# Kernel tuning notes

Hardware: AMD Instinct MI355X
Metric: run time of the kernel (lower is better)

## Reference

```python
import jax, jax.numpy as jnp
import numpy as np

V, D, H, HD, L, T, B = 65, 384, 6, 64, 6, 256, 64
EPS = 1e-3  # keras LayerNormalization default epsilon


def setup_inputs() -> dict:
    key = jax.random.key(0)
    ks = jax.random.split(key, 12)
    s = 0.02
    n = lambda k, shp: jax.random.normal(k, shp, dtype=jnp.float32) * s
    return {
        "idx": jax.random.randint(ks[0], (B, T), 0, V),
        "tok_emb": n(ks[1], (V, D)),
        "pos_emb": n(ks[2], (T, D)),
        "Wq": n(ks[3], (L, H, D, HD)),
        "Wk": n(ks[4], (L, H, D, HD)),
        "Wv": n(ks[5], (L, H, D, HD)),
        "Wproj": n(ks[6], (L, D, D)),
        "bproj": jnp.zeros((L, D), jnp.float32),
        "W1": n(ks[7], (L, D, 4 * D)),
        "b1": jnp.zeros((L, 4 * D), jnp.float32),
        "W2": n(ks[8], (L, 4 * D, D)),
        "b2": jnp.zeros((L, D), jnp.float32),
        "ln1_g": jnp.ones((L, D), jnp.float32),
        "ln1_b": jnp.zeros((L, D), jnp.float32),
        "ln2_g": jnp.ones((L, D), jnp.float32),
        "ln2_b": jnp.zeros((L, D), jnp.float32),
        "lnf_g": jnp.ones((D,), jnp.float32),
        "lnf_b": jnp.zeros((D,), jnp.float32),
        "Whead": n(ks[9], (D, V)),
        "bhead": jnp.zeros((V,), jnp.float32),
    }


def _ln(x, g, b):
    m = jnp.mean(x, axis=-1, keepdims=True)
    v = jnp.mean(jnp.square(x - m), axis=-1, keepdims=True)
    return (x - m) * jax.lax.rsqrt(v + EPS) * g + b


def reference(idx, tok_emb, pos_emb, Wq, Wk, Wv, Wproj, bproj, W1, b1, W2, b2,
              ln1_g, ln1_b, ln2_g, ln2_b, lnf_g, lnf_b, Whead, bhead):
    Bn, Tn = idx.shape
    x = tok_emb[idx] + pos_emb[:Tn]  # [B,T,D]
    mask = jnp.tril(jnp.ones((Tn, Tn), dtype=bool))
    scale = jnp.float32(D) ** -0.5  # NOTE: original scales by full C=n_embd, not head_size
    for l in range(L):
        h = _ln(x, ln1_g[l], ln1_b[l])
        q = jnp.einsum('btd,hdk->bhtk', h, Wq[l])
        k = jnp.einsum('btd,hdk->bhtk', h, Wk[l])
        v = jnp.einsum('btd,hdk->bhtk', h, Wv[l])
        wei = jnp.einsum('bhtk,bhsk->bhts', q, k) * scale
        wei = jnp.where(mask, wei, -jnp.inf)
        wei = jax.nn.softmax(wei, axis=-1)
        att = jnp.einsum('bhts,bhsk->bhtk', wei, v)
        att = att.transpose(0, 2, 1, 3).reshape(Bn, Tn, D)  # concat heads
        x = x + att @ Wproj[l] + bproj[l]
        h2 = _ln(x, ln2_g[l], ln2_b[l])
        x = x + jax.nn.relu(h2 @ W1[l] + b1[l]) @ W2[l] + b2[l]
    x = _ln(x, lnf_g, lnf_b)
    return x @ Whead + bhead  # logits [B,T,V]
```

## Files before the change

kernel.cpp:

```cpp
#include <hip/hip_runtime.h>
#include <hip/hip_bf16.h>

#define B_  64
#define T_  256
#define D_  384
#define H_  6
#define HD_ 64
#define L_  6
#define V_  65
#define BT  (B_*T_)

typedef __hip_bfloat16 bf16;
typedef unsigned short u16;
typedef short s16;
typedef __attribute__((ext_vector_type(8))) short bf16x8;
typedef __attribute__((ext_vector_type(4))) float f32x4;

#define OFF_QKV   0
#define OFF_PROJ  442368
#define OFF_W1T   589824
#define OFF_W2T   1179648
#define OFF_BPROJ 1769472
#define OFF_B1    1769856
#define OFF_B2    1771392
#define OFF_LN1G  1771776
#define OFF_LN1B  1772160
#define OFF_LN2G  1772544
#define OFF_LN2B  1772928
#define WBUF_E    1773312
#define HOFF_WHT  0
#define HOFF_BH   24960
#define HOFF_LNFG 25088
#define HOFF_LNFB 25472
#define HBUF_E    25856

__device__ __forceinline__ float u2f(u16 u) {
  union { unsigned i; float f; } c; c.i = ((unsigned)u) << 16; return c.f;
}
__device__ __forceinline__ bf16 f2b(float x) { return __float2bfloat16(x); }
__device__ __forceinline__ float b2f(bf16 x) { return __bfloat162float(x); }
__device__ __forceinline__ u16 f2u(float x) { bf16 h = f2b(x); return *(u16*)&h; }

__device__ __forceinline__ float pload(const void* p, size_t i, bool f32w) {
  return f32w ? ((const float*)p)[i] : u2f(((const u16*)p)[i]);
}

__device__ __forceinline__ void swz(int gid, int ntc, int mtiles,
                                    int& nt, int& mblk) {
  if ((mtiles & 7) == 0) {
    int per = ntc << 3;
    int g   = gid / per;
    int rem = gid - g * per;
    nt   = rem >> 3;
    mblk = (g << 3) + (rem & 7);
  } else {
    nt   = gid / mtiles;
    mblk = gid - nt * mtiles;
  }
}

__global__ __launch_bounds__(256) void detect_kernel(
    const void* p1,  const void* p2,  const void* p3,  const void* p4,
    const void* p5,  const void* p6,  const void* p7,  const void* p8,
    const void* p9,  const void* p10, const void* p11, const void* p12,
    const void* p13, const void* p14, const void* p15, const void* p16,
    const void* p17, const void* p18, const void* p19,
    const int* __restrict__ idx, unsigned* flags)
{
  const void* ps[20] = {nullptr, p1, p2, p3, p4, p5, p6, p7, p8, p9, p10,
                        p11, p12, p13, p14, p15, p16, p17, p18, p19};
  const int esz[20] = {16384, 24960, 98304, 884736, 884736, 884736, 884736,
                       2304, 3538944, 9216, 3538944, 2304, 2304, 2304, 2304,
                       2304, 384, 384, 24960, 65};
  __shared__ int r1[256], r2[256];
  int bid = blockIdx.x, tid = threadIdx.x;
  if (bid == 19) {
    int z = 0;
    for (int m = tid; m < 4096; m += 256) z += (idx[2 * m + 1] == 0) ? 1 : 0;
    r1[tid] = z; __syncthreads();
    for (int s = 128; s > 0; s >>= 1) {
      if (tid < s) r1[tid] += r1[tid + s];
      __syncthreads();
    }
    if (tid == 0) flags[20] = (r1[0] >= 4000) ? 1u : 0u;
    return;
  }
  int j = bid + 1;
  const u16* p = (const u16*)ps[j];
  int ns = esz[j] / 2; if (ns > 1024) ns = 1024;
  int band = 0, nz = 0;
  for (int i = tid; i < ns; i += 256) {
    u16 lo = p[2 * i], hi = p[2 * i + 1];
    int e = (lo >> 7) & 0xFF;
    band += (e >= 100 && e <= 127) ? 1 : 0;
    nz   += (lo | hi) ? 1 : 0;
  }
  r1[tid] = band; r2[tid] = nz; __syncthreads();
  for (int s = 128; s > 0; s >>= 1) {
    if (tid < s) { r1[tid] += r1[tid + s]; r2[tid] += r2[tid + s]; }
    __syncthreads();
  }
  if (tid == 0) flags[j] = (r2[0] > 0 && r1[0] * 2 < ns) ? 1u : 0u;
}

__global__ void const_kernel(float* out, int n, float val) {
  int i = blockIdx.x * 256 + threadIdx.x;
  if (i < n) out[i] = val;
}

__global__ __launch_bounds__(256) void conv_layer(
    const void* Wq, const void* Wk, const void* Wv, const void* Wproj,
    const void* bproj, const void* W1, const void* b1, const void* W2,
    const void* b2, const void* ln1g, const void* ln1b, const void* ln2g,
    const void* ln2b, const unsigned* __restrict__ flags,
    bf16* __restrict__ dst, int l)
{
  int e = blockIdx.x * 256 + threadIdx.x;
  if (e >= WBUF_E) return;
  float v;
  if (e < OFF_PROJ) {
    int math = e / 24576;
    int rem  = e - math * 24576;
    int hd = rem / 384, d = rem - hd * 384;
    int mat = math / 6, hh = math - mat * 6;
    const void* src = (mat == 0 ? Wq : mat == 1 ? Wk : Wv);
    v = pload(src, ((size_t)(l * 6 + hh) * 384 + d) * 64 + hd, flags[3 + mat] != 0);
  } else if (e < OFF_W1T) {
    int e2 = e - OFF_PROJ;
    int n = e2 / 384, d = e2 - n * 384;
    v = pload(Wproj, ((size_t)l * 384 + d) * 384 + n, flags[6] != 0);
  } else if (e < OFF_W2T) {
    int e2 = e - OFF_W1T;
    int n = e2 / 384, d = e2 - n * 384;
    v = pload(W1, ((size_t)l * 384 + d) * 1536 + n, flags[8] != 0);
  } else if (e < OFF_BPROJ) {
    int e2 = e - OFF_W2T;
    int n = e2 / 1536, k = e2 - n * 1536;
    v = pload(W2, ((size_t)l * 1536 + k) * 384 + n, flags[10] != 0);
  } else {
    int e2 = e - OFF_BPROJ;
    if      (e2 < 384)  v = pload(bproj, (size_t)l * 384 + e2, flags[7] != 0);
    else if (e2 < 1920) v = pload(b1, (size_t)l * 1536 + (e2 - 384), flags[9] != 0);
    else if (e2 < 2304) v = pload(b2, (size_t)l * 384 + (e2 - 1920), flags[11] != 0);
    else if (e2 < 2688) v = pload(ln1g, (size_t)l * 384 + (e2 - 2304), flags[12] != 0);
    else if (e2 < 3072) v = pload(ln1b, (size_t)l * 384 + (e2 - 2688), flags[13] != 0);
    else if (e2 < 3456) v = pload(ln2g, (size_t)l * 384 + (e2 - 3072), flags[14] != 0);
    else                v = pload(ln2b, (size_t)l * 384 + (e2 - 3456), flags[15] != 0);
  }
  dst[e] = f2b(v);
}

__global__ __launch_bounds__(256) void conv_head(
    const void* Wh, const void* bh, const void* lnfg, const void* lnfb,
    const unsigned* __restrict__ flags, bf16* __restrict__ dst)
{
  int e = blockIdx.x * 256 + threadIdx.x;
  if (e >= HBUF_E) return;
  float v = 0.f;
  if (e < HOFF_BH) {
    int n = e / 384, d = e - n * 384;
    v = pload(Wh, (size_t)d * 65 + n, flags[18] != 0);
  } else if (e < 25025) {
    v = pload(bh, e - HOFF_BH, flags[19] != 0);
  } else if (e < HOFF_LNFG) {
    v = 0.f;
  } else if (e < HOFF_LNFB) {
    v = pload(lnfg, e - HOFF_LNFG, flags[16] != 0);
  } else {
    v = pload(lnfb, e - HOFF_LNFB, flags[17] != 0);
  }
  dst[e] = f2b(v);
}

__global__ __launch_bounds__(256) void embed_kernel(
    const void* __restrict__ idx, const void* __restrict__ tok,
    const void* __restrict__ pos, bf16* __restrict__ x,
    const unsigned* __restrict__ flags)
{
  int i   = blockIdx.x * 256 + threadIdx.x;
  int tkn = i / D_;
  int d   = i - tkn * D_;
  int t   = tkn & (T_ - 1);
  long long tix;
  if (flags[20]) tix = ((const long long*)idx)[tkn];
  else           tix = ((const int*)idx)[tkn];
  float v = pload(tok, (size_t)tix * D_ + d, flags[1] != 0)
          + pload(pos, (size_t)t * D_ + d, flags[2] != 0);
  x[i] = f2b(v);
}

__global__ __launch_bounds__(256) void lnw_kernel(
    const bf16* __restrict__ x, const u16* __restrict__ g,
    const u16* __restrict__ b, bf16* __restrict__ hc, int tok0)
{
  int w = threadIdx.x >> 6, lane = threadIdx.x & 63;
  int lm = blockIdx.x * 4 + w;
  const bf16* xr = x + (size_t)(tok0 + lm) * D_;
  float v[6]; float s = 0.f;
#pragma unroll
  for (int j = 0; j < 6; j++) { v[j] = b2f(xr[lane + 64 * j]); s += v[j]; }
#pragma unroll
  for (int o = 1; o < 64; o <<= 1) s += __shfl_xor(s, o, 64);
  float mean = s * (1.0f / D_);
  float sq = 0.f;
#pragma unroll
  for (int j = 0; j < 6; j++) { float d0 = v[j] - mean; sq += d0 * d0; }
#pragma unroll
  for (int o = 1; o < 64; o <<= 1) sq += __shfl_xor(sq, o, 64);
  float inv = 1.0f / sqrtf(sq * (1.0f / D_) + 1e-3f);
  bf16* hr = hc + (size_t)lm * D_;
#pragma unroll
  for (int j = 0; j < 6; j++) {
    int d = lane + 64 * j;
    hr[d] = f2b((v[j] - mean) * inv * u2f(g[d]) + u2f(b[d]));
  }
}

__device__ __forceinline__ void gll16(const void* g, void* l) {
  __builtin_amdgcn_global_load_lds(
      (const __attribute__((address_space(1))) unsigned*)g,
      (__attribute__((address_space(3))) unsigned*)l, 16, 0, 0);
}

__device__ __forceinline__ bf16x8 ldfrag(const s16* lds, int r, int s) {
  return *(const bf16x8*)(lds + r * 64 + ((s ^ (r & 7)) << 3));
}

template<int NT, class Epi>
__device__ __forceinline__ void mcore(
    s16* __restrict__ As, s16* __restrict__ Wl,
    const u16* __restrict__ A, const u16* __restrict__ WT,
    int N, int K, int arow0, int n0, Epi epi)
{
  constexpr int MREP = (NT == 128) ? 4 : 2;
  constexpr int WPW  = NT / 32;
  int tid = threadIdx.x;
  int w = tid >> 6, lane = tid & 63;
  int quad = lane >> 4, l15 = lane & 15;
  int r8 = lane >> 3;
  int sl = ((lane & 7) ^ r8) * 8;
  int wm = (NT == 128) ? ((w >> 1) * 64) : (w * 32);
  int wn = (NT == 128) ? ((w & 1) * 64) : 0;

  f32x4 acc[MREP][4];
#pragma unroll
  for (int i = 0; i < MREP; i++)
#pragma unroll
    for (int j = 0; j < 4; j++) acc[i][j] = (f32x4){0.f, 0.f, 0.f, 0.f};

  const u16* Ag[4];
#pragma unroll
  for (int i = 0; i < 4; i++)
    Ag[i] = A + (size_t)(arow0 + (w * 4 + i) * 8 + r8) * K + sl;
  const u16* Wg[WPW];
#pragma unroll
  for (int i = 0; i < WPW; i++)
    Wg[i] = WT + (size_t)(n0 + (w * WPW + i) * 8 + r8) * K + sl;

  for (int k0 = 0; k0 < K; k0 += 64) {
    __syncthreads();
#pragma unroll
    for (int i = 0; i < 4; i++)
      gll16(Ag[i] + k0, As + (w * 4 + i) * 512);
#pragma unroll
    for (int i = 0; i < WPW; i++)
      gll16(Wg[i] + k0, Wl + (w * WPW + i) * 512);
    __syncthreads();
#pragma unroll
    for (int kh = 0; kh < 2; kh++) {
      bf16x8 am[MREP], bn[4];
#pragma unroll
      for (int i = 0; i < MREP; i++)
        am[i] = ldfrag(As, wm + i * 16 + l15, kh * 4 + quad);
#pragma unroll
      for (int j = 0; j < 4; j++)
        bn[j] = ldfrag(Wl, wn + j * 16 + l15, kh * 4 + quad);
#pragma unroll
      for (int i = 0; i < MREP; i++)
#pragma unroll
        for (int j = 0; j < 4; j++)
          acc[i][j] = __builtin_amdgcn_mfma_f32_16x16x32_bf16(am[i], bn[j], acc[i][j], 0, 0, 0);
    }
  }

#pragma unroll
  for (int i = 0; i < MREP; i++)
#pragma unroll
    for (int j = 0; j < 4; j++)
#pragma unroll
      for (int r = 0; r < 4; r++) {
        int m = wm + i * 16 + quad * 4 + r;
        int n = n0 + wn + j * 16 + l15;
        if (n < N) epi(m, n, acc[i][j][r]);
      }
}

__global__ __launch_bounds__(256) void qkv128(
    const bf16* hc, const bf16* Wbuf, bf16* qkvc, int MCa, int mtiles)
{
  __shared__ __attribute__((aligned(16))) s16 As[128 * 64];
  __shared__ __attribute__((aligned(16))) s16 Ws[128 * 64];
  int nt, mblk;
  swz(blockIdx.x, 9, mtiles, nt, mblk);
  int n0 = nt * 128, mloc0 = mblk * 128;
  auto epi = [&](int m, int n, float v) {
    int mat = n / 384;
    int rem = n - mat * 384;
    int hh = rem >> 6, hd = rem & 63;
    qkvc[(size_t)mat * MCa * D_ + (size_t)hh * MCa * HD_
         + (size_t)(mloc0 + m) * HD_ + hd] = f2b(v);
  };
  mcore<128>(As, Ws, (const u16*)hc,
             (const u16*)Wbuf + OFF_QKV, 1152, D_, mloc0, n0, epi);
}

__global__ __launch_bounds__(256) void ffn1_128(
    const bf16* hc, const bf16* Wbuf, bf16* midc, int mtiles)
{
  __shared__ __attribute__((aligned(16))) s16 As[128 * 64];
  __shared__ __attribute__((aligned(16))) s16 Ws[128 * 64];
  int nt, mblk;
  swz(blockIdx.x, 12, mtiles, nt, mblk);
  int n0 = nt * 128, m0 = mblk * 128;
  const bf16* bias = (const bf16*)Wbuf + OFF_B1;
  auto epi = [&](int m, int n, float v) {
    float r = v + b2f(bias[n]);
    midc[(size_t)(m0 + m) * (4 * D_) + n] = f2b(fmaxf(r, 0.f));
  };
  mcore<128>(As, Ws, (const u16*)hc,
             (const u16*)Wbuf + OFF_W1T, 4 * D_, D_, m0, n0, epi);
}

__global__ __launch_bounds__(256) void proj_mfma(
    const bf16* A, const bf16* Wbuf, bf16* x, int tok0, int mtiles)
{
  __shared__ __attribute__((aligned(16))) s16 As[128 * 64];
  __shared__ __attribute__((aligned(16))) s16 Ws[64 * 64];
  int nt, mblk;
  swz(blockIdx.x, 6, mtiles, nt, mblk);
  int n0 = nt * 64, m0 = mblk * 128;
  const bf16* bias = (const bf16*)Wbuf + OFF_BPROJ;
  auto epi = [&](int m, int n, float v) {
    size_t o = (size_t)(tok0 + m0 + m) * D_ + n;
    x[o] = f2b(v + b2f(bias[n]) + b2f(x[o]));
  };
  mcore<64>(As, Ws, (const u16*)A,
            (const u16*)Wbuf + OFF_PROJ, D_, D_, m0, n0, epi);
}

__global__ __launch_bounds__(256) void ffn2_mfma(
    const bf16* midc, const bf16* Wbuf, bf16* x, int tok0, int mtiles)
{
  __shared__ __attribute__((aligned(16))) s16 As[128 * 64];
  __shared__ __attribute__((aligned(16))) s16 Ws[64 * 64];
  int nt, mblk;
  swz(blockIdx.x, 6, mtiles, nt, mblk);
  int n0 = nt * 64, m0 = mblk * 128;
  const bf16* bias = (const bf16*)Wbuf + OFF_B2;
  auto epi = [&](int m, int n, float v) {
    size_t o = (size_t)(tok0 + m0 + m) * D_ + n;
    x[o] = f2b(v + b2f(bias[n]) + b2f(x[o]));
  };
  mcore<64>(As, Ws, (const u16*)midc,
            (const u16*)Wbuf + OFF_W2T, D_, 4 * D_, m0, n0, epi);
}

__global__ __launch_bounds__(256) void head_mfma(
    const bf16* hc, const bf16* Hbuf, float* out, int tok0)
{
  __shared__ __attribute__((aligned(16))) s16 As[128 * 64];
  __shared__ __attribute__((aligned(16))) s16 Ws[64 * 64];
  int n0 = blockIdx.x * 64, m0 = blockIdx.y * 128;
  const bf16* bias = (const bf16*)Hbuf + HOFF_BH;
  auto epi = [&](int m, int n, float v) {
    out[(size_t)(tok0 + m0 + m) * V_ + n] = v + b2f(bias[n]);
  };
  mcore<64>(As, Ws, (const u16*)hc,
            (const u16*)Hbuf + HOFF_WHT, V_, D_, m0, n0, epi);
}

__global__ __launch_bounds__(256) void attn4_kernel(
    const bf16* __restrict__ Q, const bf16* __restrict__ K,
    const bf16* __restrict__ V, bf16* __restrict__ att, int MCa)
{
  __shared__ s16 Qs[64 * 72];
  __shared__ s16 Ks[64 * 72];
  __shared__ __attribute__((aligned(16))) s16 Vt[64 * 64];
  __shared__ s16 Ps[4][16 * 72];
  const float scale = 0.05103103630798288f;
  int tid = threadIdx.x;
  int w = tid >> 6, lane = tid & 63;
  int quad = lane >> 4, l15 = lane & 15;
  int bid = blockIdx.x;
  int qt = bid & 3;
  int bh = bid >> 2;
  int b = bh / H_, h = bh - b * H_;
  size_t base = ((size_t)h * MCa + (size_t)b * T_) * HD_;
  int q0 = qt * 64;
  int cq = qt;

  int rstg = (tid & 7) + 8 * (tid >> 6);
  int sstg = (tid >> 3) & 7;

#pragma unroll
  for (int i = 0; i < 2; i++) {
    int r = rstg + 32 * i;
    *(bf16x8*)&Qs[r * 72 + sstg * 8] =
        *(const bf16x8*)((const u16*)Q + base + (size_t)(q0 + r) * HD_ + sstg * 8);
  }

  float mrow[4] = {-1e30f, -1e30f, -1e30f, -1e30f};
  float lrow[4] = {0.f, 0.f, 0.f, 0.f};
  f32x4 O[4];
#pragma unroll
  for (int nt = 0; nt < 4; nt++) O[nt] = (f32x4){0.f, 0.f, 0.f, 0.f};

  for (int c = 0; c <= cq; c++) {
    __syncthreads();
#pragma unroll
    for (int i = 0; i < 2; i++) {
      int r = rstg + 32 * i;
      *(bf16x8*)&Ks[r * 72 + sstg * 8] =
          *(const bf16x8*)((const u16*)K + base + (size_t)(c * 64 + r) * HD_ + sstg * 8);
      bf16x8 vv =
          *(const bf16x8*)((const u16*)V + base + (size_t)(c * 64 + r) * HD_ + sstg * 8);
      int rs = r >> 3, rl = r & 7;
      int so = ((rs ^ sstg) << 3) + rl;
#pragma unroll
      for (int k = 0; k < 8; k++)
        Vt[(sstg * 8 + k) * 64 + so] = vv[k];
    }
    __syncthreads();

    f32x4 S[4];
#pragma unroll
    for (int nt = 0; nt < 4; nt++) S[nt] = (f32x4){0.f, 0.f, 0.f, 0.f};
#pragma unroll
    for (int ks = 0; ks < 2; ks++) {
      int kk = ks * 32 + quad * 8;
      bf16x8 a = *(const bf16x8*)&Qs[(w * 16 + l15) * 72 + kk];
#pragma unroll
      for (int nt = 0; nt < 4; nt++) {
        bf16x8 bb8 = *(const bf16x8*)&Ks[(nt * 16 + l15) * 72 + kk];
        S[nt] = __builtin_amdgcn_mfma_f32_16x16x32_bf16(a, bb8, S[nt], 0, 0, 0);
      }
    }

#pragma unroll
    for (int nt = 0; nt < 4; nt++)
#pragma unroll
      for (int r = 0; r < 4; r++) {
        int qrow = q0 + w * 16 + quad * 4 + r;
        int sg = c * 64 + nt * 16 + l15;
        float v = S[nt][r] * scale;
        S[nt][r] = (sg <= qrow) ? v : -1e30f;
      }

    float alpha[4];
#pragma unroll
    for (int r = 0; r < 4; r++) {
      float mc = fmaxf(fmaxf(S[0][r], S[1][r]), fmaxf(S[2][r], S[3][r]));
#pragma unroll
      for (int o = 1; o < 16; o <<= 1) mc = fmaxf(mc, __shfl_xor(mc, o, 64));
      float mn = fmaxf(mrow[r], mc);
      alpha[r] = __expf(mrow[r] - mn);
      mrow[r] = mn;
      float s = 0.f;
#pragma unroll
      for (int nt = 0; nt < 4; nt++) {
        float p = __expf(S[nt][r] - mn);
        S[nt][r] = p;
        s += p;
      }
#pragma unroll
      for (int o = 1; o < 16; o <<= 1) s += __shfl_xor(s, o, 64);
      lrow[r] = lrow[r] * alpha[r] + s;
    }
#pragma unroll
    for (int nt = 0; nt < 4; nt++)
#pragma unroll
      for (int r = 0; r < 4; r++) O[nt][r] *= alpha[r];

#pragma unroll
    for (int nt = 0; nt < 4; nt++)
#pragma unroll
      for (int r = 0; r < 4; r++)
        Ps[w][(quad * 4 + r) * 72 + nt * 16 + l15] = (s16)f2u(S[nt][r]);
    __syncthreads();
#pragma unroll
    for (int ks = 0; ks < 2; ks++) {
      bf16x8 a = *(const bf16x8*)&Ps[w][l15 * 72 + ks * 32 + quad * 8];
#pragma unroll
      for (int nt = 0; nt < 4; nt++) {
        int d = nt * 16 + l15;
        bf16x8 bb8 = *(const bf16x8*)&Vt[d * 64 +
            (((ks * 4 + quad) ^ ((d >> 3) & 7)) << 3)];
        O[nt] = __builtin_amdgcn_mfma_f32_16x16x32_bf16(a, bb8, O[nt], 0, 0, 0);
      }
    }
  }

#pragma unroll
  for (int r = 0; r < 4; r++) {
    float invl = 1.0f / lrow[r];
#pragma unroll
    for (int nt = 0; nt < 4; nt++) {
      int qrow = q0 + w * 16 + quad * 4 + r;
      att[(size_t)(b * T_ + qrow) * D_ + h * HD_ + nt * 16 + l15] =
          f2b(O[nt][r] * invl);
    }
  }
}

extern "C" void kernel_launch(void* const* d_in, const int* in_sizes, int n_in,
                              void* d_out, int out_size, void* d_ws, size_t ws_size,
                              hipStream_t stream)
{
  float* out = (float*)d_out;
  dim3 blk(256);
  int outg = (out_size + 255) / 256;

  static const int expected[20] = {
      16384, 24960, 98304, 884736, 884736, 884736, 884736, 2304,
      3538944, 9216, 3538944, 2304, 2304, 2304, 2304, 2304, 384, 384,
      24960, 65};
  if (n_in != 20) { const_kernel<<<outg, blk, 0, stream>>>(out, out_size, 5.0f); return; }
  for (int i = 0; i < 20; i++)
    if (in_sizes[i] != expected[i]) {
      const_kernel<<<outg, blk, 0, stream>>>(out, out_size, 10.0f * (i + 1));
      return;
    }
  if (out_size != BT * V_) { const_kernel<<<outg, blk, 0, stream>>>(out, out_size, 7.0f); return; }

  const void* idx   = d_in[0];
  const void* tok   = d_in[1];
  const void* pos   = d_in[2];
  const void* Wq    = d_in[3];
  const void* Wk    = d_in[4];
  const void* Wv    = d_in[5];
  const void* Wproj = d_in[6];
  const void* bproj = d_in[7];
  const void* W1    = d_in[8];
  const void* b1    = d_in[9];
  const void* W2    = d_in[10];
  const void* b2    = d_in[11];
  const void* ln1g  = d_in[12];
  const void* ln1b  = d_in[13];
  const void* ln2g  = d_in[14];
  const void* ln2b  = d_in[15];
  const void* lnfg  = d_in[16];
  const void* lnfb  = d_in[17];
  const void* Whead = d_in[18];
  const void* bhead = d_in[19];

  const size_t off_x  = 256;
  const size_t off_wb = off_x + (size_t)BT * D_ * 2;
  const size_t off_hb = off_wb + (size_t)WBUF_E * 2;
  const size_t fixed  = off_hb + ((size_t)HBUF_E * 2 + 63) / 64 * 64;
  if (ws_size < fixed) {
    const_kernel<<<outg, blk, 0, stream>>>(out, out_size, 0.0f);
    return;
  }
  size_t region = ws_size - fixed;

  int nc = 0;
  const int candn[7] = {1, 2, 4, 8, 16, 32, 64};
  for (int i = 0; i < 7; i++)
    if ((size_t)5 * (BT / candn[i]) * D_ * 2 <= region) { nc = candn[i]; break; }
  if (!nc) { const_kernel<<<outg, blk, 0, stream>>>(out, out_size, 0.0f); return; }
  const int MCc = BT / nc;
  const int CBc = MCc / T_;
  const int mtiles = MCc / 128;

  char* wsb = (char*)d_ws;
  unsigned* flags = (unsigned*)wsb;
  bf16*   x    = (bf16*)(wsb + off_x);
  bf16*   Wbuf = (bf16*)(wsb + off_wb);
  bf16*   Hbuf = (bf16*)(wsb + off_hb);
  bf16*   hc   = (bf16*)(wsb + fixed);
  bf16*   qkvc = hc + (size_t)MCc * D_;
  bf16*   attc = qkvc + (size_t)3 * MCc * D_;
  bf16*   midc = qkvc;

  detect_kernel<<<dim3(20), blk, 0, stream>>>(
      tok, pos, Wq, Wk, Wv, Wproj, bproj, W1, b1, W2, b2,
      ln1g, ln1b, ln2g, ln2b, lnfg, lnfb, Whead, bhead,
      (const int*)idx, flags);
  embed_kernel<<<dim3(BT * D_ / 256), blk, 0, stream>>>(idx, tok, pos, x, flags);
  conv_head<<<dim3((HBUF_E + 255) / 256), blk, 0, stream>>>(
      Whead, bhead, lnfg, lnfb, flags, Hbuf);

  for (int l = 0; l < L_; l++) {
    conv_layer<<<dim3((WBUF_E + 255) / 256), blk, 0, stream>>>(
        Wq, Wk, Wv, Wproj, bproj, W1, b1, W2, b2,
        ln1g, ln1b, ln2g, ln2b, flags, Wbuf, l);
    for (int c = 0; c < nc; c++) {
      int tok0 = c * MCc;
      lnw_kernel<<<dim3(MCc / 4), blk, 0, stream>>>(
          x, (const u16*)Wbuf + OFF_LN1G, (const u16*)Wbuf + OFF_LN1B, hc, tok0);
      qkv128<<<dim3(9 * mtiles), blk, 0, stream>>>(hc, Wbuf, qkvc, MCc, mtiles);
      attn4_kernel<<<dim3(CBc * H_ * 4), blk, 0, stream>>>(
          qkvc, qkvc + (size_t)MCc * D_, qkvc + (size_t)2 * MCc * D_, attc, MCc);
      proj_mfma<<<dim3(6 * mtiles), blk, 0, stream>>>(attc, Wbuf, x, tok0, mtiles);
    }
    for (int f = 0; f < nc; f++) {
      int tok0 = f * MCc;
      lnw_kernel<<<dim3(MCc / 4), blk, 0, stream>>>(
          x, (const u16*)Wbuf + OFF_LN2G, (const u16*)Wbuf + OFF_LN2B, hc, tok0);
      ffn1_128<<<dim3(12 * mtiles), blk, 0, stream>>>(hc, Wbuf, midc, mtiles);
      ffn2_mfma<<<dim3(6 * mtiles), blk, 0, stream>>>(midc, Wbuf, x, tok0, mtiles);
    }
  }

  for (int c = 0; c < nc; c++) {
    int tok0 = c * MCc;
    lnw_kernel<<<dim3(MCc / 4), blk, 0, stream>>>(
        x, (const u16*)Hbuf + HOFF_LNFG, (const u16*)Hbuf + HOFF_LNFB, hc, tok0);
    head_mfma<<<dim3(2, MCc / 128), blk, 0, stream>>>(hc, Hbuf, out, tok0);
  }
}
```

Measured before the change: 1.134 ms.

## Double-buffer GEMM tiles in LDS and unify all GEMMs to 128x128 tiles

The shared GEMM core now prefetches the next K-slice into a second LDS buffer while MFMAs run on the current one, removing one barrier per iteration and overlapping global loads with compute. All GEMMs, including proj, ffn2 and head, now use 128x128 tiles, which halves the proj/ffn2 grids and covers the head's 65 columns with a single tile. This doubles LDS per block to 64KB, which may reduce occupancy. The smaller proj/ffn2 grids may underfill the GPU when the token chunk is small.

New measurement: 1.340 ms. +18.1%, slower.

```diff
diff --git a/kernel.cpp b/kernel.cpp
--- a/kernel.cpp
+++ b/kernel.cpp
@@ -226,25 +226,24 @@
   return *(const bf16x8*)(lds + r * 64 + ((s ^ (r & 7)) << 3));
 }
 
-template<int NT, class Epi>
+#define TBUF (128 * 64)
+
+template<class Epi>
 __device__ __forceinline__ void mcore(
     s16* __restrict__ As, s16* __restrict__ Wl,
     const u16* __restrict__ A, const u16* __restrict__ WT,
     int N, int K, int arow0, int n0, Epi epi)
 {
-  constexpr int MREP = (NT == 128) ? 4 : 2;
-  constexpr int WPW  = NT / 32;
   int tid = threadIdx.x;
   int w = tid >> 6, lane = tid & 63;
   int quad = lane >> 4, l15 = lane & 15;
   int r8 = lane >> 3;
   int sl = ((lane & 7) ^ r8) * 8;
-  int wm = (NT == 128) ? ((w >> 1) * 64) : (w * 32);
-  int wn = (NT == 128) ? ((w & 1) * 64) : 0;
-
-  f32x4 acc[MREP][4];
-#pragma unroll
-  for (int i = 0; i < MREP; i++)
+  int wm = (w >> 1) * 64, wn = (w & 1) * 64;
+
+  f32x4 acc[4][4];
+#pragma unroll
+  for (int i = 0; i < 4; i++)
 #pragma unroll
     for (int j = 0; j < 4; j++) acc[i][j] = (f32x4){0.f, 0.f, 0.f, 0.f};
 
@@ -252,39 +251,51 @@
 #pragma unroll
   for (int i = 0; i < 4; i++)
     Ag[i] = A + (size_t)(arow0 + (w * 4 + i) * 8 + r8) * K + sl;
-  const u16* Wg[WPW];
-#pragma unroll
-  for (int i = 0; i < WPW; i++)
-    Wg[i] = WT + (size_t)(n0 + (w * WPW + i) * 8 + r8) * K + sl;
-
-  for (int k0 = 0; k0 < K; k0 += 64) {
+  const u16* Wg[4];
+#pragma unroll
+  for (int i = 0; i < 4; i++)
+    Wg[i] = WT + (size_t)(n0 + (w * 4 + i) * 8 + r8) * K + sl;
+
+  int nk = K >> 6;
+#pragma unroll
+  for (int i = 0; i < 4; i++) gll16(Ag[i], As + (w * 4 + i) * 512);
+#pragma unroll
+  for (int i = 0; i < 4; i++) gll16(Wg[i], Wl + (w * 4 + i) * 512);
+
+  int cur = 0;
+  for (int t = 0; t < nk; t++) {
     __syncthreads();
-#pragma unroll
-    for (int i = 0; i < 4; i++)
-      gll16(Ag[i] + k0, As + (w * 4 + i) * 512);
-#pragma unroll
-    for (int i = 0; i < WPW; i++)
-      gll16(Wg[i] + k0, Wl + (w * WPW + i) * 512);
-    __syncthreads();
+    if (t + 1 < nk) {
+      int k0 = (t + 1) << 6;
+      s16* An = As + (cur ^ 1) * TBUF;
+      s16* Wn = Wl + (cur ^ 1) * TBUF;
+#pragma unroll
+      for (int i = 0; i < 4; i++) gll16(Ag[i] + k0, An + (w * 4 + i) * 512);
+#pragma unroll
+      for (int i = 0; i < 4; i++) gll16(Wg[i] + k0, Wn + (w * 4 + i) * 512);
+    }
+    const s16* Ab = As + cur * TBUF;
+    const s16* Wb = Wl + cur * TBUF;
 #pragma unroll
     for (int kh = 0; kh < 2; kh++) {
-      bf16x8 am[MREP], bn[4];
-#pragma unroll
-      for (int i = 0; i < MREP; i++)
-        am[i] = ldfrag(As, wm + i * 16 + l15, kh * 4 + quad);
+      bf16x8 am[4], bn[4];
+#pragma unroll
+      for (int i = 0; i < 4; i++)
+        am[i] = ldfrag(Ab, wm + i * 16 + l15, kh * 4 + quad);
 #pragma unroll
       for (int j = 0; j < 4; j++)
-        bn[j] = ldfrag(Wl, wn + j * 16 + l15, kh * 4 + quad);
-#pragma unroll
-      for (int i = 0; i < MREP; i++)
+        bn[j] = ldfrag(Wb, wn + j * 16 + l15, kh * 4 + quad);
+#pragma unroll
+      for (int i = 0; i < 4; i++)
 #pragma unroll
         for (int j = 0; j < 4; j++)
           acc[i][j] = __builtin_amdgcn_mfma_f32_16x16x32_bf16(am[i], bn[j], acc[i][j], 0, 0, 0);
     }
-  }
-
-#pragma unroll
-  for (int i = 0; i < MREP; i++)
+    cur ^= 1;
+  }
+
+#pragma unroll
+  for (int i = 0; i < 4; i++)
 #pragma unroll
     for (int j = 0; j < 4; j++)
 #pragma unroll
@@ -295,11 +306,14 @@
       }
 }
 
+#define MCORE_LDS \
+  __shared__ __attribute__((aligned(16))) s16 As[2 * TBUF]; \
+  __shared__ __attribute__((aligned(16))) s16 Ws[2 * TBUF];
+
 __global__ __launch_bounds__(256) void qkv128(
     const bf16* hc, const bf16* Wbuf, bf16* qkvc, int MCa, int mtiles)
 {
-  __shared__ __attribute__((aligned(16))) s16 As[128 * 64];
-  __shared__ __attribute__((aligned(16))) s16 Ws[128 * 64];
+  MCORE_LDS
   int nt, mblk;
   swz(blockIdx.x, 9, mtiles, nt, mblk);
   int n0 = nt * 128, mloc0 = mblk * 128;
@@ -310,15 +324,14 @@
     qkvc[(size_t)mat * MCa * D_ + (size_t)hh * MCa * HD_
          + (size_t)(mloc0 + m) * HD_ + hd] = f2b(v);
   };
-  mcore<128>(As, Ws, (const u16*)hc,
-             (const u16*)Wbuf + OFF_QKV, 1152, D_, mloc0, n0, epi);
+  mcore(As, Ws, (const u16*)hc,
+        (const u16*)Wbuf + OFF_QKV, 1152, D_, mloc0, n0, epi);
 }
 
 __global__ __launch_bounds__(256) void ffn1_128(
     const bf16* hc, const bf16* Wbuf, bf16* midc, int mtiles)
 {
-  __shared__ __attribute__((aligned(16))) s16 As[128 * 64];
-  __shared__ __attribute__((aligned(16))) s16 Ws[128 * 64];
+  MCORE_LDS
   int nt, mblk;
   swz(blockIdx.x, 12, mtiles, nt, mblk);
   int n0 = nt * 128, m0 = mblk * 128;
@@ -327,56 +340,53 @@
     float r = v + b2f(bias[n]);
     midc[(size_t)(m0 + m) * (4 * D_) + n] = f2b(fmaxf(r, 0.f));
   };
-  mcore<128>(As, Ws, (const u16*)hc,
-             (const u16*)Wbuf + OFF_W1T, 4 * D_, D_, m0, n0, epi);
+  mcore(As, Ws, (const u16*)hc,
+        (const u16*)Wbuf + OFF_W1T, 4 * D_, D_, m0, n0, epi);
 }
 
 __global__ __launch_bounds__(256) void proj_mfma(
     const bf16* A, const bf16* Wbuf, bf16* x, int tok0, int mtiles)
 {
-  __shared__ __attribute__((aligned(16))) s16 As[128 * 64];
-  __shared__ __attribute__((aligned(16))) s16 Ws[64 * 64];
+  MCORE_LDS
   int nt, mblk;
-  swz(blockIdx.x, 6, mtiles, nt, mblk);
-  int n0 = nt * 64, m0 = mblk * 128;
+  swz(blockIdx.x, 3, mtiles, nt, mblk);
+  int n0 = nt * 128, m0 = mblk * 128;
   const bf16* bias = (const bf16*)Wbuf + OFF_BPROJ;
   auto epi = [&](int m, int n, float v) {
     size_t o = (size_t)(tok0 + m0 + m) * D_ + n;
     x[o] = f2b(v + b2f(bias[n]) + b2f(x[o]));
   };
-  mcore<64>(As, Ws, (const u16*)A,
-            (const u16*)Wbuf + OFF_PROJ, D_, D_, m0, n0, epi);
+  mcore(As, Ws, (const u16*)A,
+        (const u16*)Wbuf + OFF_PROJ, D_, D_, m0, n0, epi);
 }
 
 __global__ __launch_bounds__(256) void ffn2_mfma(
     const bf16* midc, const bf16* Wbuf, bf16* x, int tok0, int mtiles)
 {
-  __shared__ __attribute__((aligned(16))) s16 As[128 * 64];
-  __shared__ __attribute__((aligned(16))) s16 Ws[64 * 64];
+  MCORE_LDS
   int nt, mblk;
-  swz(blockIdx.x, 6, mtiles, nt, mblk);
-  int n0 = nt * 64, m0 = mblk * 128;
+  swz(blockIdx.x, 3, mtiles, nt, mblk);
+  int n0 = nt * 128, m0 = mblk * 128;
   const bf16* bias = (const bf16*)Wbuf + OFF_B2;
   auto epi = [&](int m, int n, float v) {
     size_t o = (size_t)(tok0 + m0 + m) * D_ + n;
     x[o] = f2b(v + b2f(bias[n]) + b2f(x[o]));
   };
-  mcore<64>(As, Ws, (const u16*)midc,
-            (const u16*)Wbuf + OFF_W2T, D_, 4 * D_, m0, n0, epi);
+  mcore(As, Ws, (const u16*)midc,
+        (const u16*)Wbuf + OFF_W2T, D_, 4 * D_, m0, n0, epi);
 }
 
 __global__ __launch_bounds__(256) void head_mfma(
     const bf16* hc, const bf16* Hbuf, float* out, int tok0)
 {
-  __shared__ __attribute__((aligned(16))) s16 As[128 * 64];
-  __shared__ __attribute__((aligned(16))) s16 Ws[64 * 64];
-  int n0 = blockIdx.x * 64, m0 = blockIdx.y * 128;
+  MCORE_LDS
+  int m0 = blockIdx.x * 128;
   const bf16* bias = (const bf16*)Hbuf + HOFF_BH;
   auto epi = [&](int m, int n, float v) {
     out[(size_t)(tok0 + m0 + m) * V_ + n] = v + b2f(bias[n]);
   };
-  mcore<64>(As, Ws, (const u16*)hc,
-            (const u16*)Hbuf + HOFF_WHT, V_, D_, m0, n0, epi);
+  mcore(As, Ws, (const u16*)hc,
+        (const u16*)Hbuf + HOFF_WHT, V_, D_, m0, 0, epi);
 }
 
 __global__ __launch_bounds__(256) void attn4_kernel(
@@ -601,14 +611,14 @@
       qkv128<<<dim3(9 * mtiles), blk, 0, stream>>>(hc, Wbuf, qkvc, MCc, mtiles);
       attn4_kernel<<<dim3(CBc * H_ * 4), blk, 0, stream>>>(
           qkvc, qkvc + (size_t)MCc * D_, qkvc + (size_t)2 * MCc * D_, attc, MCc);
-      proj_mfma<<<dim3(6 * mtiles), blk, 0, stream>>>(attc, Wbuf, x, tok0, mtiles);
+      proj_mfma<<<dim3(3 * mtiles), blk, 0, stream>>>(attc, Wbuf, x, tok0, mtiles);
     }
     for (int f = 0; f < nc; f++) {
       int tok0 = f * MCc;
       lnw_kernel<<<dim3(MCc / 4), blk, 0, stream>>>(
           x, (const u16*)Wbuf + OFF_LN2G, (const u16*)Wbuf + OFF_LN2B, hc, tok0);
       ffn1_128<<<dim3(12 * mtiles), blk, 0, stream>>>(hc, Wbuf, midc, mtiles);
-      ffn2_mfma<<<dim3(6 * mtiles), blk, 0, stream>>>(midc, Wbuf, x, tok0, mtiles);
+      ffn2_mfma<<<dim3(3 * mtiles), blk, 0, stream>>>(midc, Wbuf, x, tok0, mtiles);
     }
   }
 
@@ -616,6 +626,6 @@
     int tok0 = c * MCc;
     lnw_kernel<<<dim3(MCc / 4), blk, 0, stream>>>(
         x, (const u16*)Hbuf + HOFF_LNFG, (const u16*)Hbuf + HOFF_LNFB, hc, tok0);
-    head_mfma<<<dim3(2, MCc / 128), blk, 0, stream>>>(hc, Hbuf, out, tok0);
-  }
-}
+    head_mfma<<<dim3(MCc / 128), blk, 0, stream>>>(hc, Hbuf, out, tok0);
+  }
+}
```
